# Optimization experiments

Hardware: AMD Instinct MI355X
Metric: run time of the kernel (lower is better)

## Reference

```python
import jax, jax.numpy as jnp
import numpy as np

NUM_HEADS = 16

def _apply_rope(x, cos, sin):
    # x: (B, H, T, D); cos/sin: (T, D//2)
    B, H, T, D = x.shape
    xr = x.reshape(B, H, T, D // 2, 2)
    x0, x1 = xr[..., 0], xr[..., 1]
    c = cos[None, None, :, :]
    s = sin[None, None, :, :]
    out = jnp.stack([x0 * c - x1 * s, x0 * s + x1 * c], axis=-1)
    return out.reshape(B, H, T, D)


def setup_inputs() -> dict:
    key = jax.random.key(0)
    k1, k2, k3 = jax.random.split(key, 3)
    B, T, C = 2, 2048, 1024
    D = C // NUM_HEADS
    x = jax.random.normal(k1, (B, T, C), dtype=jnp.float32)
    qkv_w = jax.random.normal(k2, (3 * C, C), dtype=jnp.float32) * (C ** -0.5)
    proj_w = jax.random.normal(k3, (C, C), dtype=jnp.float32) * (C ** -0.5)
    # standard RoPE frequency table (theta = 10000)
    inv_freq = 1.0 / (10000.0 ** (jnp.arange(0, D, 2, dtype=jnp.float32) / D))  # (D/2,)
    angles = jnp.arange(T, dtype=jnp.float32)[:, None] * inv_freq[None, :]      # (T, D/2)
    return {
        "x": x,
        "freqs_cos": jnp.cos(angles),
        "freqs_sin": jnp.sin(angles),
        "qkv_w": qkv_w,
        "proj_w": proj_w,
    }


def reference(x, freqs_cos, freqs_sin, qkv_w, proj_w):
    B, T, C = x.shape
    H = NUM_HEADS
    D = C // H
    qkv = x @ qkv_w.T                                  # (B, T, 3C)
    q, k, v = jnp.split(qkv, 3, axis=-1)
    q = q.reshape(B, T, H, D).transpose(0, 2, 1, 3)    # (B, H, T, D)
    k = k.reshape(B, T, H, D).transpose(0, 2, 1, 3)
    v = v.reshape(B, T, H, D).transpose(0, 2, 1, 3)
    q = _apply_rope(q, freqs_cos, freqs_sin)
    k = _apply_rope(k, freqs_cos, freqs_sin)
    scale = 1.0 / jnp.sqrt(jnp.asarray(D, dtype=x.dtype))
    scores = jnp.einsum('bhqd,bhkd->bhqk', q, k) * scale
    causal = jnp.tril(jnp.ones((T, T), dtype=bool))
    scores = jnp.where(causal[None, None], scores, jnp.finfo(scores.dtype).min)
    attn = jax.nn.softmax(scores, axis=-1)
    out = jnp.einsum('bhqk,bhkd->bhqd', attn, v)       # (B, H, T, D)
    out = out.transpose(0, 2, 1, 3).reshape(B, T, C)
    return out @ proj_w.T
```

## Files before the change

### kernel.cpp

```cpp
#include <hip/hip_runtime.h>
#include <stdint.h>

#define DI __device__ __forceinline__

typedef unsigned short u16;
typedef __bf16 bf16x8 __attribute__((ext_vector_type(8)));
typedef unsigned short u16x8 __attribute__((ext_vector_type(8)));
typedef unsigned short u16x4 __attribute__((ext_vector_type(4)));
typedef float f32x4 __attribute__((ext_vector_type(4)));

DI u16 f2bf(float f) { __bf16 h = (__bf16)f; return __builtin_bit_cast(u16, h); }
DI float bf2f(u16 u) { return (float)__builtin_bit_cast(__bf16, u); }

DI bf16x8 ld8(const u16* p) { return __builtin_bit_cast(bf16x8, *(const u16x8*)p); }

DI f32x4 mfma16(bf16x8 a, bf16x8 b, f32x4 c) {
  return __builtin_amdgcn_mfma_f32_16x16x32_bf16(a, b, c, 0, 0, 0);
}

DI void async16(const u16* g, u16* l) {
  __builtin_amdgcn_global_load_lds((const __attribute__((address_space(1))) void*)g,
                                   (__attribute__((address_space(3))) void*)l, 16, 0, 0);
}

__global__ __launch_bounds__(256) void cast_bf16_k(const float* __restrict__ in,
                                                   u16* __restrict__ out) {
  const int i = blockIdx.x * 256 + threadIdx.x;
  const float4 v = ((const float4*)in)[i];
  u16x4 o = {f2bf(v.x), f2bf(v.y), f2bf(v.z), f2bf(v.w)};
  ((u16x4*)out)[i] = o;
}

template <int OUT_BF16>
__global__ __launch_bounds__(256) void gemm_bt(const u16* __restrict__ A,
                                               const u16* __restrict__ W,
                                               void* __restrict__ outp,
                                               int M, int N, int K) {
  __shared__ u16 sA[128 * 32];
  __shared__ u16 sB[128 * 32];
  const int tid = threadIdx.x;
  const int w = tid >> 6, L = tid & 63;
  const int lo = L & 15, quad = L >> 4;
  const int nb = N >> 7;
  const int bm = blockIdx.x / nb, bn = blockIdx.x - bm * nb;
  const int m0 = bm << 7, n0 = bn << 7;
  const int wm = (w >> 1) << 6, wn = (w & 1) << 6;

  f32x4 acc[4][4];
#pragma unroll
  for (int i = 0; i < 4; ++i)
#pragma unroll
    for (int j = 0; j < 4; ++j) acc[i][j] = 0.f;

  const int r0 = tid >> 2, s0 = tid & 3;
  const int c0 = s0 ^ ((r0 >> 1) & 3);
  const int r1 = r0 + 64;
  const int c1 = s0 ^ ((r1 >> 1) & 3);
  const size_t aRow0 = (size_t)(m0 + r0) * K, aRow1 = (size_t)(m0 + r1) * K;
  const size_t bRow0 = (size_t)(n0 + r0) * K, bRow1 = (size_t)(n0 + r1) * K;

  int raf[4], rbf[4];
#pragma unroll
  for (int mt = 0; mt < 4; ++mt) {
    int r = wm + mt * 16 + lo;
    raf[mt] = r * 32 + ((quad ^ ((r >> 1) & 3)) << 3);
    r = wn + mt * 16 + lo;
    rbf[mt] = r * 32 + ((quad ^ ((r >> 1) & 3)) << 3);
  }

  const int kIters = K >> 5;
  for (int kt = 0; kt < kIters; ++kt) {
    const int kb = kt << 5;
    async16(A + aRow0 + kb + c0 * 8, &sA[tid * 8]);
    async16(A + aRow1 + kb + c1 * 8, &sA[(tid + 256) * 8]);
    async16(W + bRow0 + kb + c0 * 8, &sB[tid * 8]);
    async16(W + bRow1 + kb + c1 * 8, &sB[(tid + 256) * 8]);
    __syncthreads();
    bf16x8 af[4], bfr[4];
#pragma unroll
    for (int mt = 0; mt < 4; ++mt) af[mt] = ld8(&sA[raf[mt]]);
#pragma unroll
    for (int nt = 0; nt < 4; ++nt) bfr[nt] = ld8(&sB[rbf[nt]]);
#pragma unroll
    for (int mt = 0; mt < 4; ++mt)
#pragma unroll
      for (int nt = 0; nt < 4; ++nt)
        acc[mt][nt] = mfma16(af[mt], bfr[nt], acc[mt][nt]);
    __syncthreads();
  }

#pragma unroll
  for (int mt = 0; mt < 4; ++mt) {
    const int m = m0 + wm + mt * 16 + quad * 4;
#pragma unroll
    for (int nt = 0; nt < 4; ++nt) {
      const int n = n0 + wn + nt * 16 + lo;
#pragma unroll
      for (int r = 0; r < 4; ++r) {
        const size_t off = (size_t)(m + r) * N + n;
        if (OUT_BF16)
          ((u16*)outp)[off] = f2bf(acc[mt][nt][r]);
        else
          ((float*)outp)[off] = acc[mt][nt][r];
      }
    }
  }
}

__global__ __launch_bounds__(256) void rope_k(const u16* __restrict__ qkv,
                                              const float* __restrict__ cosb,
                                              const float* __restrict__ sinb,
                                              u16* __restrict__ qo, u16* __restrict__ ko) {
  const int idx = blockIdx.x * 256 + threadIdx.x;
  const int i = idx & 31;
  const int t = (idx >> 5) & 2047;
  const int h = (idx >> 16) & 15;
  const int b = idx >> 20;
  const size_t src = ((size_t)(b * 2048 + t)) * 3072 + h * 64 + 2 * i;
  const float q0v = bf2f(qkv[src]), q1v = bf2f(qkv[src + 1]);
  const float k0v = bf2f(qkv[src + 1024]), k1v = bf2f(qkv[src + 1025]);
  const float c = cosb[t * 32 + i], s = sinb[t * 32 + i];
  const size_t dst = ((size_t)((b * 16 + h) * 2048 + t)) * 64 + 2 * i;
  qo[dst] = f2bf((q0v * c - q1v * s) * 0.125f);
  qo[dst + 1] = f2bf((q0v * s + q1v * c) * 0.125f);
  ko[dst] = f2bf(k0v * c - k1v * s);
  ko[dst + 1] = f2bf(k0v * s + k1v * c);
}

__global__ __launch_bounds__(256) void vt_k(const u16* __restrict__ qkv,
                                            u16* __restrict__ vt) {
  __shared__ u16 sT[64 * 64];
  const int tid = threadIdx.x;
  const int bh = blockIdx.x & 31;
  const int t0 = (blockIdx.x >> 5) << 6;
  const int b = bh >> 4, h = bh & 15;
#pragma unroll
  for (int it = 0; it < 2; ++it) {
    const int id = tid + it * 256;
    const int tr = id >> 3, s = id & 7, c = s ^ (tr & 7);
    async16(qkv + (size_t)(b * 2048 + t0 + tr) * 3072 + 2048 + h * 64 + c * 8, &sT[id * 8]);
  }
  __syncthreads();
#pragma unroll
  for (int it = 0; it < 2; ++it) {
    const int id = tid + it * 256;
    const int d = id >> 3, ct = id & 7;
    u16x8 o;
#pragma unroll
    for (int j = 0; j < 8; ++j) {
      const int t = ct * 8 + j;
      o[j] = sT[t * 64 + (((d >> 3) ^ (t & 7)) << 3) + (d & 7)];
    }
    *(u16x8*)(vt + ((size_t)bh * 64 + d) * 2048 + t0 + ct * 8) = o;
  }
}

__global__ __launch_bounds__(256) void fattn(const u16* __restrict__ qs,
                                             const u16* __restrict__ ks,
                                             const u16* __restrict__ vt,
                                             u16* __restrict__ aout) {
  __shared__ u16 sK[64 * 64];
  __shared__ u16 sVt[64 * 64];
  __shared__ u16 sP[4][16 * 64];
  const int tid = threadIdx.x;
  const int w = tid >> 6, L = tid & 63;
  const int lo = L & 15, quad = L >> 4;
  const int bh = blockIdx.x & 31;
  const int qi = 31 - (blockIdx.x >> 5);
  const size_t hoff = (size_t)bh * (2048 * 64);
  const int q0 = qi << 6;
  const int wq = q0 + w * 16;
  u16* sPw = sP[w];

  bf16x8 qb[2];
#pragma unroll
  for (int kd = 0; kd < 2; ++kd)
    qb[kd] = ld8(qs + hoff + (size_t)(wq + lo) * 64 + kd * 32 + quad * 8);

  float m_s = -3.0e38f, l_s = 0.f;
  f32x4 ot[4];
#pragma unroll
  for (int mt = 0; mt < 4; ++mt) ot[mt] = 0.f;

  const int ntiles = qi + 1;
  for (int kt = 0; kt < ntiles; ++kt) {
    const int kv0 = kt << 6;
#pragma unroll
    for (int it = 0; it < 2; ++it) {
      const int id = tid + it * 256;
      const int kv = id >> 3, s = id & 7, c = s ^ (kv & 7);
      async16(ks + hoff + (size_t)(kv0 + kv) * 64 + c * 8, &sK[id * 8]);
    }
#pragma unroll
    for (int it = 0; it < 2; ++it) {
      const int id = tid + it * 256;
      const int d = id >> 3, s = id & 7, c = s ^ (d & 7);
      async16(vt + hoff + (size_t)d * 2048 + kv0 + c * 8, &sVt[id * 8]);
    }
    __syncthreads();

    f32x4 st[4];
#pragma unroll
    for (int mt = 0; mt < 4; ++mt) st[mt] = 0.f;
#pragma unroll
    for (int mt = 0; mt < 4; ++mt) {
      const int kv = mt * 16 + lo;
#pragma unroll
      for (int kd = 0; kd < 2; ++kd) {
        const int c = kd * 4 + quad;
        bf16x8 ka = ld8(&sK[kv * 64 + ((c ^ (kv & 7)) << 3)]);
        st[mt] = mfma16(ka, qb[kd], st[mt]);
      }
    }
    if (kt == qi) {
      const int qg = wq + lo;
#pragma unroll
      for (int mt = 0; mt < 4; ++mt)
#pragma unroll
        for (int r = 0; r < 4; ++r) {
          const int kvg = kv0 + mt * 16 + quad * 4 + r;
          if (kvg > qg) st[mt][r] = -3.0e38f;
        }
    }
    float mx = -3.0e38f;
#pragma unroll
    for (int mt = 0; mt < 4; ++mt)
#pragma unroll
      for (int r = 0; r < 4; ++r) mx = fmaxf(mx, st[mt][r]);
    mx = fmaxf(mx, __shfl_xor(mx, 16));
    mx = fmaxf(mx, __shfl_xor(mx, 32));
    const float mnew = fmaxf(m_s, mx);
    const float alpha = __expf(m_s - mnew);
    float rs = 0.f;
#pragma unroll
    for (int mt = 0; mt < 4; ++mt)
#pragma unroll
      for (int r = 0; r < 4; ++r) {
        float p = __expf(st[mt][r] - mnew);
        p = bf2f(f2bf(p));
        st[mt][r] = p;
        rs += p;
      }
    rs += __shfl_xor(rs, 16);
    rs += __shfl_xor(rs, 32);
    l_s = l_s * alpha + rs;
    m_s = mnew;
#pragma unroll
    for (int mt = 0; mt < 4; ++mt) {
      u16x4 pk = {f2bf(st[mt][0]), f2bf(st[mt][1]), f2bf(st[mt][2]), f2bf(st[mt][3])};
      const int c2 = 2 * mt + (quad >> 1);
      *(u16x4*)&sPw[lo * 64 + ((c2 ^ (lo & 7)) << 3) + (quad & 1) * 4] = pk;
    }
#pragma unroll
    for (int mt = 0; mt < 4; ++mt)
#pragma unroll
      for (int r = 0; r < 4; ++r) ot[mt][r] *= alpha;
    asm volatile("s_waitcnt lgkmcnt(0)" ::: "memory");
    bf16x8 pbf[2];
#pragma unroll
    for (int kh = 0; kh < 2; ++kh) {
      const int c = kh * 4 + quad;
      pbf[kh] = ld8(&sPw[lo * 64 + ((c ^ (lo & 7)) << 3)]);
    }
#pragma unroll
    for (int mt = 0; mt < 4; ++mt) {
      const int d = mt * 16 + lo;
#pragma unroll
      for (int kh = 0; kh < 2; ++kh) {
        const int c = kh * 4 + quad;
        bf16x8 va = ld8(&sVt[d * 64 + ((c ^ (d & 7)) << 3)]);
        ot[mt] = mfma16(va, pbf[kh], ot[mt]);
      }
    }
    __syncthreads();
  }

  const float iv = 1.f / l_s;
#pragma unroll
  for (int mt = 0; mt < 4; ++mt) {
    u16x4 ok = {f2bf(ot[mt][0] * iv), f2bf(ot[mt][1] * iv), f2bf(ot[mt][2] * iv),
                f2bf(ot[mt][3] * iv)};
    const int c2 = 2 * mt + (quad >> 1);
    *(u16x4*)&sPw[lo * 64 + ((c2 ^ (lo & 7)) << 3) + (quad & 1) * 4] = ok;
  }
  asm volatile("s_waitcnt lgkmcnt(0)" ::: "memory");
  const int b = bh >> 4, h = bh & 15;
#pragma unroll
  for (int rr = 0; rr < 2; ++rr) {
    const int q = rr * 8 + (L >> 3);
    const int cd = L & 7;
    u16x8 o8 = *(const u16x8*)&sPw[q * 64 + ((cd ^ (q & 7)) << 3)];
    const int t = wq + q;
    *(u16x8*)(aout + ((size_t)(b * 2048 + t)) * 1024 + h * 64 + cd * 8) = o8;
  }
}

extern "C" void kernel_launch(void* const* d_in, const int* in_sizes, int n_in,
                              void* d_out, int out_size, void* d_ws, size_t ws_size,
                              hipStream_t stream) {
  const float* x = (const float*)d_in[0];
  const float* fcos = (const float*)d_in[1];
  const float* fsin = (const float*)d_in[2];
  const float* qkvw = (const float*)d_in[3];
  const float* projw = (const float*)d_in[4];
  float* out = (float*)d_out;

  char* ws = (char*)d_ws;
  u16* x_bf = (u16*)(ws);
  u16* qkvw_bf = (u16*)(ws + (8u << 20));
  u16* projw_bf = (u16*)(ws + (14u << 20));
  u16* qkv_bf = (u16*)(ws + (16u << 20));
  u16* q_bf = (u16*)(ws + (40u << 20));
  u16* k_bf = (u16*)(ws + (48u << 20));
  u16* vt = (u16*)(ws + (56u << 20));
  u16* attn_bf = (u16*)(ws + (64u << 20));

  cast_bf16_k<<<4096, 256, 0, stream>>>(x, x_bf);
  cast_bf16_k<<<3072, 256, 0, stream>>>(qkvw, qkvw_bf);
  cast_bf16_k<<<1024, 256, 0, stream>>>(projw, projw_bf);
  gemm_bt<1><<<768, 256, 0, stream>>>(x_bf, qkvw_bf, (void*)qkv_bf, 4096, 3072, 1024);
  rope_k<<<8192, 256, 0, stream>>>(qkv_bf, fcos, fsin, q_bf, k_bf);
  vt_k<<<1024, 256, 0, stream>>>(qkv_bf, vt);
  fattn<<<1024, 256, 0, stream>>>(q_bf, k_bf, vt, attn_bf);
  gemm_bt<0><<<256, 256, 0, stream>>>(attn_bf, projw_bf, (void*)out, 4096, 1024, 1024);
}
```

Measured before the change: 204.7 us.

## Double-buffer LDS in GEMM and attention, fold log2e into Q scale

Both the GEMM and the flash-attention kernels now use two LDS buffers. The next tile's async global-to-LDS load is issued right after the barrier, so it can overlap the MFMA work on the current tile, and one barrier per iteration is dropped. The Q scale now includes log2(e), so the softmax can use the raw exp2 instruction instead of __expf. The bf16 round-trip on p before the row sum is also removed. This doubles LDS use per block, which may lower occupancy, and it relies on a single barrier per iteration to guard buffer reuse.

```diff
diff --git a/kernel.cpp b/kernel.cpp
--- a/kernel.cpp
+++ b/kernel.cpp
@@ -36,8 +36,8 @@
                                                const u16* __restrict__ W,
                                                void* __restrict__ outp,
                                                int M, int N, int K) {
-  __shared__ u16 sA[128 * 32];
-  __shared__ u16 sB[128 * 32];
+  __shared__ u16 sA[2 * 4096];
+  __shared__ u16 sB[2 * 4096];
   const int tid = threadIdx.x;
   const int w = tid >> 6, L = tid & 63;
   const int lo = L & 15, quad = L >> 4;
@@ -68,25 +68,30 @@
     rbf[mt] = r * 32 + ((quad ^ ((r >> 1) & 3)) << 3);
   }
 
+  auto stage = [&](int kb, int buf) {
+    const int bo = buf << 12;
+    async16(A + aRow0 + kb + c0 * 8, &sA[bo + tid * 8]);
+    async16(A + aRow1 + kb + c1 * 8, &sA[bo + (tid + 256) * 8]);
+    async16(W + bRow0 + kb + c0 * 8, &sB[bo + tid * 8]);
+    async16(W + bRow1 + kb + c1 * 8, &sB[bo + (tid + 256) * 8]);
+  };
+
   const int kIters = K >> 5;
+  stage(0, 0);
   for (int kt = 0; kt < kIters; ++kt) {
-    const int kb = kt << 5;
-    async16(A + aRow0 + kb + c0 * 8, &sA[tid * 8]);
-    async16(A + aRow1 + kb + c1 * 8, &sA[(tid + 256) * 8]);
-    async16(W + bRow0 + kb + c0 * 8, &sB[tid * 8]);
-    async16(W + bRow1 + kb + c1 * 8, &sB[(tid + 256) * 8]);
     __syncthreads();
+    if (kt + 1 < kIters) stage((kt + 1) << 5, (kt + 1) & 1);
+    const int bo = (kt & 1) << 12;
     bf16x8 af[4], bfr[4];
 #pragma unroll
-    for (int mt = 0; mt < 4; ++mt) af[mt] = ld8(&sA[raf[mt]]);
-#pragma unroll
-    for (int nt = 0; nt < 4; ++nt) bfr[nt] = ld8(&sB[rbf[nt]]);
+    for (int mt = 0; mt < 4; ++mt) af[mt] = ld8(&sA[bo + raf[mt]]);
+#pragma unroll
+    for (int nt = 0; nt < 4; ++nt) bfr[nt] = ld8(&sB[bo + rbf[nt]]);
 #pragma unroll
     for (int mt = 0; mt < 4; ++mt)
 #pragma unroll
       for (int nt = 0; nt < 4; ++nt)
         acc[mt][nt] = mfma16(af[mt], bfr[nt], acc[mt][nt]);
-    __syncthreads();
   }
 
 #pragma unroll
@@ -107,6 +112,7 @@
   }
 }
 
+#define QSCALE 0.18033688011112f
 __global__ __launch_bounds__(256) void rope_k(const u16* __restrict__ qkv,
                                               const float* __restrict__ cosb,
                                               const float* __restrict__ sinb,
@@ -121,8 +127,8 @@
   const float k0v = bf2f(qkv[src + 1024]), k1v = bf2f(qkv[src + 1025]);
   const float c = cosb[t * 32 + i], s = sinb[t * 32 + i];
   const size_t dst = ((size_t)((b * 16 + h) * 2048 + t)) * 64 + 2 * i;
-  qo[dst] = f2bf((q0v * c - q1v * s) * 0.125f);
-  qo[dst + 1] = f2bf((q0v * s + q1v * c) * 0.125f);
+  qo[dst] = f2bf((q0v * c - q1v * s) * QSCALE);
+  qo[dst + 1] = f2bf((q0v * s + q1v * c) * QSCALE);
   ko[dst] = f2bf(k0v * c - k1v * s);
   ko[dst + 1] = f2bf(k0v * s + k1v * c);
 }
@@ -159,8 +165,8 @@
                                              const u16* __restrict__ ks,
                                              const u16* __restrict__ vt,
                                              u16* __restrict__ aout) {
-  __shared__ u16 sK[64 * 64];
-  __shared__ u16 sVt[64 * 64];
+  __shared__ u16 sK[2 * 4096];
+  __shared__ u16 sVt[2 * 4096];
   __shared__ u16 sP[4][16 * 64];
   const int tid = threadIdx.x;
   const int w = tid >> 6, L = tid & 63;
@@ -172,32 +178,39 @@
   const int wq = q0 + w * 16;
   u16* sPw = sP[w];
 
-  bf16x8 qb[2];
-#pragma unroll
-  for (int kd = 0; kd < 2; ++kd)
-    qb[kd] = ld8(qs + hoff + (size_t)(wq + lo) * 64 + kd * 32 + quad * 8);
-
-  float m_s = -3.0e38f, l_s = 0.f;
-  f32x4 ot[4];
-#pragma unroll
-  for (int mt = 0; mt < 4; ++mt) ot[mt] = 0.f;
-
-  const int ntiles = qi + 1;
-  for (int kt = 0; kt < ntiles; ++kt) {
-    const int kv0 = kt << 6;
+  auto stage = [&](int kv0, int buf) {
+    const int bo = buf << 12;
 #pragma unroll
     for (int it = 0; it < 2; ++it) {
       const int id = tid + it * 256;
       const int kv = id >> 3, s = id & 7, c = s ^ (kv & 7);
-      async16(ks + hoff + (size_t)(kv0 + kv) * 64 + c * 8, &sK[id * 8]);
+      async16(ks + hoff + (size_t)(kv0 + kv) * 64 + c * 8, &sK[bo + id * 8]);
     }
 #pragma unroll
     for (int it = 0; it < 2; ++it) {
       const int id = tid + it * 256;
       const int d = id >> 3, s = id & 7, c = s ^ (d & 7);
-      async16(vt + hoff + (size_t)d * 2048 + kv0 + c * 8, &sVt[id * 8]);
-    }
+      async16(vt + hoff + (size_t)d * 2048 + kv0 + c * 8, &sVt[bo + id * 8]);
+    }
+  };
+
+  bf16x8 qb[2];
+#pragma unroll
+  for (int kd = 0; kd < 2; ++kd)
+    qb[kd] = ld8(qs + hoff + (size_t)(wq + lo) * 64 + kd * 32 + quad * 8);
+
+  float m_s = -3.0e38f, l_s = 0.f;
+  f32x4 ot[4];
+#pragma unroll
+  for (int mt = 0; mt < 4; ++mt) ot[mt] = 0.f;
+
+  const int ntiles = qi + 1;
+  stage(0, 0);
+  for (int kt = 0; kt < ntiles; ++kt) {
     __syncthreads();
+    if (kt + 1 < ntiles) stage((kt + 1) << 6, (kt + 1) & 1);
+    const int bo = (kt & 1) << 12;
+    const int kv0 = kt << 6;
 
     f32x4 st[4];
 #pragma unroll
@@ -208,7 +221,7 @@
 #pragma unroll
       for (int kd = 0; kd < 2; ++kd) {
         const int c = kd * 4 + quad;
-        bf16x8 ka = ld8(&sK[kv * 64 + ((c ^ (kv & 7)) << 3)]);
+        bf16x8 ka = ld8(&sK[bo + kv * 64 + ((c ^ (kv & 7)) << 3)]);
         st[mt] = mfma16(ka, qb[kd], st[mt]);
       }
     }
@@ -230,14 +243,13 @@
     mx = fmaxf(mx, __shfl_xor(mx, 16));
     mx = fmaxf(mx, __shfl_xor(mx, 32));
     const float mnew = fmaxf(m_s, mx);
-    const float alpha = __expf(m_s - mnew);
+    const float alpha = __builtin_amdgcn_exp2f(m_s - mnew);
     float rs = 0.f;
 #pragma unroll
     for (int mt = 0; mt < 4; ++mt)
 #pragma unroll
       for (int r = 0; r < 4; ++r) {
-        float p = __expf(st[mt][r] - mnew);
-        p = bf2f(f2bf(p));
+        const float p = __builtin_amdgcn_exp2f(st[mt][r] - mnew);
         st[mt][r] = p;
         rs += p;
       }
@@ -268,11 +280,10 @@
 #pragma unroll
       for (int kh = 0; kh < 2; ++kh) {
         const int c = kh * 4 + quad;
-        bf16x8 va = ld8(&sVt[d * 64 + ((c ^ (d & 7)) << 3)]);
+        bf16x8 va = ld8(&sVt[bo + d * 64 + ((c ^ (d & 7)) << 3)]);
         ot[mt] = mfma16(va, pbf[kh], ot[mt]);
       }
     }
-    __syncthreads();
   }
 
   const float iv = 1.f / l_s;
```

After: 198.5 us. 3.0% less time.
